# Kernel tuning notes

Hardware: AMD Instinct MI355X
Metric: run time of the kernel (lower is better)

Reference implementation:

```python
import jax, jax.numpy as jnp
import numpy as np

EPS = 1e-7


def setup_inputs() -> dict:
    key = jax.random.key(0)
    k1, k2, k3 = jax.random.split(key, 3)
    B, Nt, Nv, D = 64, 128, 256, 512
    text_feats = jax.random.normal(k1, (B, Nt, D), dtype=jnp.float32)
    visual_feats = jax.random.normal(k2, (B, Nv, D), dtype=jnp.float32)
    attention_mask = jax.random.randint(k3, (B, Nt), 0, 2, dtype=jnp.int32)
    return {"text_feats": text_feats, "visual_feats": visual_feats,
            "attention_mask": attention_mask}


def _l2norm(x):
    return x / jnp.clip(jnp.linalg.norm(x, axis=-1, keepdims=True), 1e-12)


def reference(text_feats, visual_feats, attention_mask):
    # Normalize token features (F.normalize along D)
    t = _l2norm(text_feats)            # (B, Nt, D)
    v = _l2norm(visual_feats)          # (B, Nv, D)
    # All-pairs token similarities: (B, B, Nt, Nv)
    token_sims = jnp.einsum('itd,jvd->ijtv', t, v)
    # Max over visual tokens -> (B, B, Nt)
    max_sims = jnp.max(token_sims, axis=3)
    # Masked mean over text tokens -> (B, B)
    mask = attention_mask.astype(jnp.float32)[:, None, :]   # (B, 1, Nt) broadcasts over pairs
    masked_sum = jnp.sum(max_sims * mask, axis=2)            # (B, B)
    valid = jnp.clip(jnp.sum(mask, axis=2), EPS)             # (B, 1)
    clip_sims = masked_sum / valid                           # (B, B)
    # Symmetric InfoNCE on the diagonal
    B = clip_sims.shape[0]
    diag = jnp.arange(B)
    losses_t2v = -jax.nn.log_softmax(clip_sims, axis=1)[diag, diag]
    losses_v2t = -jax.nn.log_softmax(clip_sims.T, axis=1)[diag, diag]
    contrastive_loss = jnp.mean(losses_t2v + losses_v2t) / 2.0
    # Regularization: keep negative token sims near zero
    neg_sims = jnp.clip(token_sims, -20.0, 0.0)
    reg_loss = 0.15 * jnp.mean(neg_sims ** 2)
    return contrastive_loss + reg_loss
```

## Files before the change

kernel.cpp:

```cpp
#include <hip/hip_runtime.h>
#include <hip/hip_bf16.h>

#define BB 64
#define NT 128
#define NV 256
#define DD 512
#define BK 32
#define EPSF 1e-7f

typedef __attribute__((ext_vector_type(8))) short bf16x8;
typedef __attribute__((ext_vector_type(4))) float f32x4;

__device__ __forceinline__ void glds16(const ushort* g, ushort* l) {
    __builtin_amdgcn_global_load_lds(
        (const __attribute__((address_space(1))) unsigned int*)g,
        (__attribute__((address_space(3))) unsigned int*)l, 16, 0, 0);
}

__global__ __launch_bounds__(256) void k_normalize(
    const float* __restrict__ tf, const float* __restrict__ vf,
    __hip_bfloat16* __restrict__ tn, __hip_bfloat16* __restrict__ vn,
    float* __restrict__ reg_sum) {
    int row = blockIdx.x;
    if (row == 0 && threadIdx.x == 0) *reg_sum = 0.0f;
    const float* src;
    __hip_bfloat16* dst;
    if (row < BB * NT) {
        src = tf + (size_t)row * DD;
        dst = tn + (size_t)row * DD;
    } else {
        int r = row - BB * NT;
        src = vf + (size_t)r * DD;
        dst = vn + (size_t)r * DD;
    }
    int tid = threadIdx.x;
    float2 x = ((const float2*)src)[tid];
    float ss = x.x * x.x + x.y * x.y;
    #pragma unroll
    for (int off = 32; off; off >>= 1) ss += __shfl_down(ss, off, 64);
    __shared__ float wsum[4];
    int lane = tid & 63, wid = tid >> 6;
    if (lane == 0) wsum[wid] = ss;
    __syncthreads();
    float tot = wsum[0] + wsum[1] + wsum[2] + wsum[3];
    float scale = 1.0f / fmaxf(sqrtf(tot), 1e-12f);
    __hip_bfloat162 o;
    o.x = __float2bfloat16(x.x * scale);
    o.y = __float2bfloat16(x.y * scale);
    ((__hip_bfloat162*)dst)[tid] = o;
}

__global__ __launch_bounds__(256, 2) void k_gemm(
    const __hip_bfloat16* __restrict__ tn, const __hip_bfloat16* __restrict__ vn,
    const int* __restrict__ mask,
    float* __restrict__ clip_sims, float* __restrict__ reg_sum) {
    __shared__ ushort sT[NT][BK];
    __shared__ ushort sV[NV][BK];
    __shared__ float maxbuf[NT][2];
    __shared__ float redw[4];
    __shared__ float c0[2], c1[2];

    const int i = blockIdx.x, j = blockIdx.y;
    const int tid = threadIdx.x;
    const int l = tid & 63, w = tid >> 6;
    const int wr = w >> 1, wc = w & 1;
    const int m15 = l & 15, q = l >> 4;

    const ushort* tbase = (const ushort*)tn + (size_t)i * NT * DD;
    const ushort* vbase = (const ushort*)vn + (size_t)j * NV * DD;

    ushort* sTf = &sT[0][0];
    ushort* sVf = &sV[0][0];

    int t_off[2], t_l[2];
    #pragma unroll
    for (int s = 0; s < 2; ++s) {
        int f = s * 256 + tid;
        int r = f >> 2, qp = f & 3;
        int qs = qp ^ ((r >> 1) & 3);
        t_off[s] = r * DD + qs * 8;
        t_l[s] = f * 8;
    }
    int v_off[4], v_l[4];
    #pragma unroll
    for (int s = 0; s < 4; ++s) {
        int f = s * 256 + tid;
        int r = f >> 2, qp = f & 3;
        int qs = qp ^ ((r >> 1) & 3);
        v_off[s] = r * DD + qs * 8;
        v_l[s] = f * 8;
    }

    int a_idx[4], b_idx[8];
    #pragma unroll
    for (int rt = 0; rt < 4; ++rt) {
        int row = wr * 64 + rt * 16 + m15;
        int qp = q ^ ((row >> 1) & 3);
        a_idx[rt] = row * BK + qp * 8;
    }
    #pragma unroll
    for (int ct = 0; ct < 8; ++ct) {
        int row = wc * 128 + ct * 16 + m15;
        int qp = q ^ ((row >> 1) & 3);
        b_idx[ct] = row * BK + qp * 8;
    }

    f32x4 acc[4][8];
    #pragma unroll
    for (int rt = 0; rt < 4; ++rt)
        #pragma unroll
        for (int ct = 0; ct < 8; ++ct) acc[rt][ct] = (f32x4){0.f, 0.f, 0.f, 0.f};

    for (int kk = 0; kk < DD; kk += BK) {
        #pragma unroll
        for (int s = 0; s < 2; ++s)
            glds16(tbase + t_off[s] + kk, sTf + t_l[s]);
        #pragma unroll
        for (int s = 0; s < 4; ++s)
            glds16(vbase + v_off[s] + kk, sVf + v_l[s]);
        __syncthreads();

        bf16x8 a[4], b[8];
        #pragma unroll
        for (int rt = 0; rt < 4; ++rt) a[rt] = *(const bf16x8*)(sTf + a_idx[rt]);
        #pragma unroll
        for (int ct = 0; ct < 8; ++ct) b[ct] = *(const bf16x8*)(sVf + b_idx[ct]);
        #pragma unroll
        for (int rt = 0; rt < 4; ++rt)
            #pragma unroll
            for (int ct = 0; ct < 8; ++ct)
                acc[rt][ct] = __builtin_amdgcn_mfma_f32_16x16x32_bf16(
                    a[rt], b[ct], acc[rt][ct], 0, 0, 0);
        __syncthreads();
    }

    float rp = 0.0f;
    #pragma unroll
    for (int rt = 0; rt < 4; ++rt)
        #pragma unroll
        for (int ct = 0; ct < 8; ++ct)
            #pragma unroll
            for (int r = 0; r < 4; ++r) {
                float m = fminf(acc[rt][ct][r], 0.0f);
                rp = fmaf(m, m, rp);
            }

    #pragma unroll
    for (int rt = 0; rt < 4; ++rt)
        #pragma unroll
        for (int r = 0; r < 4; ++r) {
            float m = acc[rt][0][r];
            #pragma unroll
            for (int ct = 1; ct < 8; ++ct) m = fmaxf(m, acc[rt][ct][r]);
            #pragma unroll
            for (int msk = 1; msk < 16; msk <<= 1)
                m = fmaxf(m, __shfl_xor(m, msk, 64));
            if (m15 == 0)
                maxbuf[wr * 64 + rt * 16 + q * 4 + r][wc] = m;
        }

    #pragma unroll
    for (int off = 32; off; off >>= 1) rp += __shfl_down(rp, off, 64);
    if (l == 0) redw[w] = rp;
    __syncthreads();

    if (tid < NT) {
        float rm = fmaxf(maxbuf[tid][0], maxbuf[tid][1]);
        float mf = (float)mask[i * NT + tid];
        float v = rm * mf;
        #pragma unroll
        for (int off = 32; off; off >>= 1) {
            v += __shfl_down(v, off, 64);
            mf += __shfl_down(mf, off, 64);
        }
        if (l == 0) { c0[w] = v; c1[w] = mf; }
    }
    __syncthreads();
    if (tid == 0) {
        clip_sims[i * BB + j] = (c0[0] + c0[1]) / fmaxf(c1[0] + c1[1], EPSF);
        atomicAdd(reg_sum, redw[0] + redw[1] + redw[2] + redw[3]);
    }
}

__global__ __launch_bounds__(256) void k_loss(
    const float* __restrict__ clip_sims, const float* __restrict__ reg_sum,
    float* __restrict__ out) {
    __shared__ float sc[BB][BB + 1];
    __shared__ float lrow[BB], lcol[BB];
    int tid = threadIdx.x;
    for (int idx = tid; idx < BB * BB; idx += 256)
        sc[idx / BB][idx % BB] = clip_sims[idx];
    __syncthreads();
    if (tid < BB) {
        int i = tid;
        float m = sc[i][0];
        #pragma unroll
        for (int j = 1; j < BB; ++j) m = fmaxf(m, sc[i][j]);
        float s = 0.0f;
        #pragma unroll
        for (int j = 0; j < BB; ++j) s += expf(sc[i][j] - m);
        lrow[i] = m + logf(s) - sc[i][i];
    } else if (tid < 2 * BB) {
        int i = tid - BB;
        float m = sc[0][i];
        #pragma unroll
        for (int j = 1; j < BB; ++j) m = fmaxf(m, sc[j][i]);
        float s = 0.0f;
        #pragma unroll
        for (int j = 0; j < BB; ++j) s += expf(sc[j][i] - m);
        lcol[i] = m + logf(s) - sc[i][i];
    }
    __syncthreads();
    if (tid == 0) {
        float tot = 0.0f;
        for (int i = 0; i < BB; ++i) tot += lrow[i] + lcol[i];
        float contrastive = tot / (2.0f * BB);
        double denom = (double)BB * BB * NT * NV;
        float reg = 0.15f * (float)((double)reg_sum[0] / denom);
        out[0] = contrastive + reg;
    }
}

extern "C" void kernel_launch(void* const* d_in, const int* in_sizes, int n_in,
                              void* d_out, int out_size, void* d_ws, size_t ws_size,
                              hipStream_t stream) {
    const float* tf = (const float*)d_in[0];
    const float* vf = (const float*)d_in[1];
    const int* mask = (const int*)d_in[2];
    float* out = (float*)d_out;

    char* ws = (char*)d_ws;
    size_t tn_bytes = (size_t)BB * NT * DD * sizeof(__hip_bfloat16);
    size_t vn_bytes = (size_t)BB * NV * DD * sizeof(__hip_bfloat16);
    size_t cs_bytes = (size_t)BB * BB * sizeof(float);

    __hip_bfloat16* tn = (__hip_bfloat16*)ws;
    __hip_bfloat16* vn = (__hip_bfloat16*)(ws + tn_bytes);
    float* clip_sims = (float*)(ws + tn_bytes + vn_bytes);
    float* reg_sum = (float*)(ws + tn_bytes + vn_bytes + cs_bytes);

    k_normalize<<<BB * NT + BB * NV, 256, 0, stream>>>(tf, vf, tn, vn, reg_sum);
    k_gemm<<<dim3(BB, BB), 256, 0, stream>>>(tn, vn, mask, clip_sims, reg_sum);
    k_loss<<<1, 256, 0, stream>>>(clip_sims, reg_sum, out);
}
```

Before: 258.5 us.

## Switch similarity GEMM to FP8 scaled MFMA with wave-per-row normalization

```diff
diff --git a/kernel.cpp b/kernel.cpp
--- a/kernel.cpp
+++ b/kernel.cpp
@@ -5,13 +5,14 @@
 #define NT 128
 #define NV 256
 #define DD 512
-#define BK 32
+#define BKB 128
 #define EPSF 1e-7f
 
-typedef __attribute__((ext_vector_type(8))) short bf16x8;
+typedef __attribute__((ext_vector_type(8))) int i32x8;
+typedef __attribute__((ext_vector_type(4))) int i32x4;
 typedef __attribute__((ext_vector_type(4))) float f32x4;
 
-__device__ __forceinline__ void glds16(const ushort* g, ushort* l) {
+__device__ __forceinline__ void glds16(const uchar* g, uchar* l) {
     __builtin_amdgcn_global_load_lds(
         (const __attribute__((address_space(1))) unsigned int*)g,
         (__attribute__((address_space(3))) unsigned int*)l, 16, 0, 0);
@@ -19,12 +20,13 @@
 
 __global__ __launch_bounds__(256) void k_normalize(
     const float* __restrict__ tf, const float* __restrict__ vf,
-    __hip_bfloat16* __restrict__ tn, __hip_bfloat16* __restrict__ vn,
+    uchar* __restrict__ tn, uchar* __restrict__ vn,
     float* __restrict__ reg_sum) {
-    int row = blockIdx.x;
-    if (row == 0 && threadIdx.x == 0) *reg_sum = 0.0f;
+    if (blockIdx.x == 0 && threadIdx.x == 0) *reg_sum = 0.0f;
+    const int w = threadIdx.x >> 6, l = threadIdx.x & 63;
+    const int row = blockIdx.x * 4 + w;
     const float* src;
-    __hip_bfloat16* dst;
+    uchar* dst;
     if (row < BB * NT) {
         src = tf + (size_t)row * DD;
         dst = tn + (size_t)row * DD;
@@ -33,29 +35,26 @@
         src = vf + (size_t)r * DD;
         dst = vn + (size_t)r * DD;
     }
-    int tid = threadIdx.x;
-    float2 x = ((const float2*)src)[tid];
-    float ss = x.x * x.x + x.y * x.y;
-    #pragma unroll
-    for (int off = 32; off; off >>= 1) ss += __shfl_down(ss, off, 64);
-    __shared__ float wsum[4];
-    int lane = tid & 63, wid = tid >> 6;
-    if (lane == 0) wsum[wid] = ss;
-    __syncthreads();
-    float tot = wsum[0] + wsum[1] + wsum[2] + wsum[3];
-    float scale = 1.0f / fmaxf(sqrtf(tot), 1e-12f);
-    __hip_bfloat162 o;
-    o.x = __float2bfloat16(x.x * scale);
-    o.y = __float2bfloat16(x.y * scale);
-    ((__hip_bfloat162*)dst)[tid] = o;
+    float4 x0 = ((const float4*)src)[l * 2];
+    float4 x1 = ((const float4*)src)[l * 2 + 1];
+    float ss = x0.x * x0.x + x0.y * x0.y + x0.z * x0.z + x0.w * x0.w
+             + x1.x * x1.x + x1.y * x1.y + x1.z * x1.z + x1.w * x1.w;
+    #pragma unroll
+    for (int off = 32; off; off >>= 1) ss += __shfl_xor(ss, off, 64);
+    float scale = 1.0f / fmaxf(sqrtf(ss), 1e-12f);
+    int p0 = __builtin_amdgcn_cvt_pk_fp8_f32(x0.x * scale, x0.y * scale, 0, 0);
+    p0 = __builtin_amdgcn_cvt_pk_fp8_f32(x0.z * scale, x0.w * scale, p0, 1);
+    int p1 = __builtin_amdgcn_cvt_pk_fp8_f32(x1.x * scale, x1.y * scale, 0, 0);
+    p1 = __builtin_amdgcn_cvt_pk_fp8_f32(x1.z * scale, x1.w * scale, p1, 1);
+    ((uint2*)dst)[l] = make_uint2((unsigned)p0, (unsigned)p1);
 }
 
 __global__ __launch_bounds__(256, 2) void k_gemm(
-    const __hip_bfloat16* __restrict__ tn, const __hip_bfloat16* __restrict__ vn,
+    const uchar* __restrict__ tn, const uchar* __restrict__ vn,
     const int* __restrict__ mask,
     float* __restrict__ clip_sims, float* __restrict__ reg_sum) {
-    __shared__ ushort sT[NT][BK];
-    __shared__ ushort sV[NV][BK];
+    __shared__ uchar sT[NT * BKB];
+    __shared__ uchar sV[NV * BKB];
     __shared__ float maxbuf[NT][2];
     __shared__ float redw[4];
     __shared__ float c0[2], c1[2];
@@ -66,43 +65,35 @@
     const int wr = w >> 1, wc = w & 1;
     const int m15 = l & 15, q = l >> 4;
 
-    const ushort* tbase = (const ushort*)tn + (size_t)i * NT * DD;
-    const ushort* vbase = (const ushort*)vn + (size_t)j * NV * DD;
-
-    ushort* sTf = &sT[0][0];
-    ushort* sVf = &sV[0][0];
-
-    int t_off[2], t_l[2];
-    #pragma unroll
-    for (int s = 0; s < 2; ++s) {
-        int f = s * 256 + tid;
-        int r = f >> 2, qp = f & 3;
-        int qs = qp ^ ((r >> 1) & 3);
-        t_off[s] = r * DD + qs * 8;
-        t_l[s] = f * 8;
-    }
-    int v_off[4], v_l[4];
+    const uchar* tbase = tn + (size_t)i * NT * DD;
+    const uchar* vbase = vn + (size_t)j * NV * DD;
+
+    int t_off[4], v_off[8];
     #pragma unroll
     for (int s = 0; s < 4; ++s) {
         int f = s * 256 + tid;
-        int r = f >> 2, qp = f & 3;
-        int qs = qp ^ ((r >> 1) & 3);
-        v_off[s] = r * DD + qs * 8;
-        v_l[s] = f * 8;
-    }
-
-    int a_idx[4], b_idx[8];
+        int r = f >> 3, p = f & 7, g = (p - r) & 7;
+        t_off[s] = r * DD + g * 16;
+    }
+    #pragma unroll
+    for (int s = 0; s < 8; ++s) {
+        int f = s * 256 + tid;
+        int r = f >> 3, p = f & 7, g = (p - r) & 7;
+        v_off[s] = r * DD + g * 16;
+    }
+
+    int a_b0[4], a_b1[4], b_b0[8], b_b1[8];
     #pragma unroll
     for (int rt = 0; rt < 4; ++rt) {
         int row = wr * 64 + rt * 16 + m15;
-        int qp = q ^ ((row >> 1) & 3);
-        a_idx[rt] = row * BK + qp * 8;
+        a_b0[rt] = row * BKB + (((2 * q + row) & 7) * 16);
+        a_b1[rt] = row * BKB + (((2 * q + 1 + row) & 7) * 16);
     }
     #pragma unroll
     for (int ct = 0; ct < 8; ++ct) {
         int row = wc * 128 + ct * 16 + m15;
-        int qp = q ^ ((row >> 1) & 3);
-        b_idx[ct] = row * BK + qp * 8;
+        b_b0[ct] = row * BKB + (((2 * q + row) & 7) * 16);
+        b_b1[ct] = row * BKB + (((2 * q + 1 + row) & 7) * 16);
     }
 
     f32x4 acc[4][8];
@@ -111,26 +102,34 @@
         #pragma unroll
         for (int ct = 0; ct < 8; ++ct) acc[rt][ct] = (f32x4){0.f, 0.f, 0.f, 0.f};
 
-    for (int kk = 0; kk < DD; kk += BK) {
-        #pragma unroll
-        for (int s = 0; s < 2; ++s)
-            glds16(tbase + t_off[s] + kk, sTf + t_l[s]);
+    for (int kk = 0; kk < DD; kk += BKB) {
         #pragma unroll
         for (int s = 0; s < 4; ++s)
-            glds16(vbase + v_off[s] + kk, sVf + v_l[s]);
+            glds16(tbase + t_off[s] + kk, sT + (s * 256 + tid) * 16);
+        #pragma unroll
+        for (int s = 0; s < 8; ++s)
+            glds16(vbase + v_off[s] + kk, sV + (s * 256 + tid) * 16);
         __syncthreads();
 
-        bf16x8 a[4], b[8];
-        #pragma unroll
-        for (int rt = 0; rt < 4; ++rt) a[rt] = *(const bf16x8*)(sTf + a_idx[rt]);
-        #pragma unroll
-        for (int ct = 0; ct < 8; ++ct) b[ct] = *(const bf16x8*)(sVf + b_idx[ct]);
-        #pragma unroll
-        for (int rt = 0; rt < 4; ++rt)
-            #pragma unroll
-            for (int ct = 0; ct < 8; ++ct)
-                acc[rt][ct] = __builtin_amdgcn_mfma_f32_16x16x32_bf16(
-                    a[rt], b[ct], acc[rt][ct], 0, 0, 0);
+        i32x8 a[4];
+        #pragma unroll
+        for (int rt = 0; rt < 4; ++rt) {
+            i32x4 lo = *(const i32x4*)(sT + a_b0[rt]);
+            i32x4 hi = *(const i32x4*)(sT + a_b1[rt]);
+            a[rt] = (i32x8){lo.x, lo.y, lo.z, lo.w, hi.x, hi.y, hi.z, hi.w};
+        }
+        #pragma unroll
+        for (int ct = 0; ct < 8; ++ct) {
+            i32x4 lo = *(const i32x4*)(sV + b_b0[ct]);
+            i32x4 hi = *(const i32x4*)(sV + b_b1[ct]);
+            i32x8 b = (i32x8){lo.x, lo.y, lo.z, lo.w, hi.x, hi.y, hi.z, hi.w};
+            #pragma unroll
+            for (int rt = 0; rt < 4; ++rt)
+                acc[rt][ct] = __builtin_amdgcn_mfma_scale_f32_16x16x128_f8f6f4(
+                    a[rt], b, acc[rt][ct],
+                    0 , 0 ,
+                    0, 127 , 0, 127 );
+        }
         __syncthreads();
     }
 
@@ -230,16 +229,16 @@
     float* out = (float*)d_out;
 
     char* ws = (char*)d_ws;
-    size_t tn_bytes = (size_t)BB * NT * DD * sizeof(__hip_bfloat16);
-    size_t vn_bytes = (size_t)BB * NV * DD * sizeof(__hip_bfloat16);
+    size_t tn_bytes = (size_t)BB * NT * DD;
+    size_t vn_bytes = (size_t)BB * NV * DD;
     size_t cs_bytes = (size_t)BB * BB * sizeof(float);
 
-    __hip_bfloat16* tn = (__hip_bfloat16*)ws;
-    __hip_bfloat16* vn = (__hip_bfloat16*)(ws + tn_bytes);
+    uchar* tn = (uchar*)ws;
+    uchar* vn = (uchar*)(ws + tn_bytes);
     float* clip_sims = (float*)(ws + tn_bytes + vn_bytes);
     float* reg_sum = (float*)(ws + tn_bytes + vn_bytes + cs_bytes);
 
-    k_normalize<<<BB * NT + BB * NV, 256, 0, stream>>>(tf, vf, tn, vn, reg_sum);
+    k_normalize<<<(BB * NT + BB * NV) / 4, 256, 0, stream>>>(tf, vf, tn, vn, reg_sum);
     k_gemm<<<dim3(BB, BB), 256, 0, stream>>>(tn, vn, mask, clip_sims, reg_sum);
     k_loss<<<1, 256, 0, stream>>>(clip_sims, reg_sum, out);
 }
```

Result: slower. 578.8 us (+123.9%).
